# Optimization experiments

Measured on AMD Instinct MI355X. Metric: run time of the kernel, lower is better.

Reference implementation:

```python
import jax, jax.numpy as jnp
import numpy as np

N_NODES = 50000
N_EDGES = 800000
IN_DIM = 64
HID = 64
N_CLASSES = 10
NUM_GRAPHS = 512
EPS = 1e-5


def setup_inputs() -> dict:
    key = jax.random.key(0)
    ks = jax.random.split(key, 24)
    def w(k, shape, fan_in):
        return jax.random.normal(k, shape, jnp.float32) / np.sqrt(fan_in)
    inp = {
        "input_feature": jax.random.normal(ks[0], (N_NODES, IN_DIM), jnp.float32),
        "edge_src": jax.random.randint(ks[1], (N_EDGES,), 0, N_NODES, jnp.int32),
        "edge_dst": jax.random.randint(ks[2], (N_EDGES,), 0, N_NODES, jnp.int32),
        "graph_indicator": jnp.sort(jax.random.randint(ks[3], (N_NODES,), 0, NUM_GRAPHS, jnp.int32)),
        "labels": jax.random.randint(ks[4], (NUM_GRAPHS,), 0, N_CLASSES, jnp.int32),
        # GraphSAGE layer weights (self + neighbor paths) and biases
        "Ws1": w(ks[5], (IN_DIM, HID), IN_DIM), "Wn1": w(ks[6], (IN_DIM, HID), IN_DIM), "b1": jnp.zeros((HID,), jnp.float32),
        "Ws2": w(ks[7], (HID, HID), HID), "Wn2": w(ks[8], (HID, HID), HID), "b2": jnp.zeros((HID,), jnp.float32),
        "Ws3": w(ks[9], (HID, HID), HID), "Wn3": w(ks[10], (HID, HID), HID), "b3": jnp.zeros((HID,), jnp.float32),
        # BatchNorm affine params (bn1 output is discarded by the original forward, so omitted)
        "g2": jnp.ones((HID,), jnp.float32), "be2": jnp.zeros((HID,), jnp.float32),
        "g3": jnp.ones((HID,), jnp.float32), "be3": jnp.zeros((HID,), jnp.float32),
        # MLP head
        "fcW1": w(ks[11], (HID, 2 * HID), HID), "fcb1": jnp.zeros((2 * HID,), jnp.float32),
        "fcW2": w(ks[12], (2 * HID, HID), 2 * HID), "fcb2": jnp.zeros((HID,), jnp.float32),
        "fcW3": w(ks[13], (HID, N_CLASSES), HID), "fcb3": jnp.zeros((N_CLASSES,), jnp.float32),
    }
    return inp


def _batchnorm(x, g, b):
    # training-mode BN over the node dimension
    m = jnp.mean(x, axis=0)
    v = jnp.var(x, axis=0)
    return (x - m) * jax.lax.rsqrt(v + EPS) * g + b


def _sage(x, Ws, Wn, b, src, dst, inv_deg):
    # mean-aggregate neighbor features: agg[i] = mean_{(j->i) in E} x[j]
    msg = x[src]                                                   # [E, d] gather
    agg = jax.ops.segment_sum(msg, dst, num_segments=N_NODES)       # [N, d] scatter-add
    agg = agg * inv_deg                                             # mean aggregation
    return jax.nn.relu(x @ Ws + agg @ Wn + b)


def reference(input_feature, edge_src, edge_dst, graph_indicator, labels,
              Ws1, Wn1, b1, Ws2, Wn2, b2, Ws3, Wn3, b3,
              g2, be2, g3, be3, fcW1, fcb1, fcW2, fcb2, fcW3, fcb3):
    deg = jax.ops.segment_sum(jnp.ones((N_EDGES,), jnp.float32), edge_dst, num_segments=N_NODES)
    inv_deg = (1.0 / jnp.maximum(deg, 1.0))[:, None]                # [N, 1]
    # NOTE: original forward computes bn1(input_feature) but discards it (dead code)
    h = _sage(input_feature, Ws1, Wn1, b1, edge_src, edge_dst, inv_deg)
    h = _batchnorm(h, g2, be2)
    h = _sage(h, Ws2, Wn2, b2, edge_src, edge_dst, inv_deg)
    h = _batchnorm(h, g3, be3)
    h = _sage(h, Ws3, Wn3, b3, edge_src, edge_dst, inv_deg)
    # sum-pool per graph (labels only determine the number of graphs)
    pooled = jax.ops.segment_sum(h, graph_indicator, num_segments=NUM_GRAPHS)  # [G, HID]
    h = jax.nn.relu(pooled @ fcW1 + fcb1)
    h = jax.nn.relu(h @ fcW2 + fcb2)
    logits = h @ fcW3 + fcb3                                        # [G, num_classes]
    return logits
```

## Files before the change

### kernel.cpp

```cpp
#include <hip/hip_runtime.h>

#define N_NODES   50000
#define N_EDGES   800000
#define DIM       64
#define NUM_GRAPHS 512
#define EPS       1e-5f

#define SB   1024
#define NSB  ((N_NODES + SB - 1) / SB)

__global__ void k_zero(int* __restrict__ deg, float* __restrict__ sums2,
                       float* __restrict__ sums3, float* __restrict__ pooled) {
    int i = blockIdx.x * 256 + threadIdx.x;
    if (i < N_NODES) deg[i] = 0;
    if (i < 128) { sums2[i] = 0.f; sums3[i] = 0.f; }
    if (i < NUM_GRAPHS * DIM) pooled[i] = 0.f;
}

__global__ void k_count(const int* __restrict__ dst, int* __restrict__ deg) {
    int i = blockIdx.x * 256 + threadIdx.x;
    if (i < N_EDGES) atomicAdd(&deg[dst[i]], 1);
}

__global__ void __launch_bounds__(1024)
k_scan1(const int* __restrict__ deg, int* __restrict__ bsum) {
    __shared__ int red[16];
    int t = threadIdx.x;
    int i = blockIdx.x * SB + t;
    int v = (i < N_NODES) ? deg[i] : 0;
#pragma unroll
    for (int d = 32; d; d >>= 1) v += __shfl_down(v, d, 64);
    if ((t & 63) == 0) red[t >> 6] = v;
    __syncthreads();
    if (t < 16) {
        int s = red[t];
#pragma unroll
        for (int d = 8; d; d >>= 1) s += __shfl_down(s, d, 16);
        if (t == 0) bsum[blockIdx.x] = s;
    }
}

__global__ void k_scan2(const int* __restrict__ bsum, int* __restrict__ boff) {
    int t = threadIdx.x;
    int v = (t < NSB) ? bsum[t] : 0;
    int orig = v;
#pragma unroll
    for (int d = 1; d < 64; d <<= 1) {
        int u = __shfl_up(v, d, 64);
        if (t >= d) v += u;
    }
    if (t < NSB) boff[t] = v - orig;
}

__global__ void __launch_bounds__(1024)
k_scan3(const int* __restrict__ deg, const int* __restrict__ boff,
        int* __restrict__ off, int* __restrict__ cursor, float* __restrict__ invd) {
    __shared__ int wsum[16];
    int t = threadIdx.x, lane = t & 63, w = t >> 6;
    int i = blockIdx.x * SB + t;
    int d = (i < N_NODES) ? deg[i] : 0;
    int v = d;
#pragma unroll
    for (int s = 1; s < 64; s <<= 1) {
        int u = __shfl_up(v, s, 64);
        if (lane >= s) v += u;
    }
    if (lane == 63) wsum[w] = v;
    __syncthreads();
    if (t < 16) {
        int x = wsum[t];
#pragma unroll
        for (int s = 1; s < 16; s <<= 1) {
            int u = __shfl_up(x, s, 16);
            if (t >= s) x += u;
        }
        wsum[t] = x;
    }
    __syncthreads();
    if (i < N_NODES) {
        int ex = boff[blockIdx.x] + ((w > 0) ? wsum[w - 1] : 0) + v - d;
        off[i] = ex;
        cursor[i] = ex;
        invd[i] = 1.0f / (float)max(d, 1);
        if (i == N_NODES - 1) off[N_NODES] = ex + d;
    }
}

__global__ void k_scatter(const int* __restrict__ src, const int* __restrict__ dst,
                          int* __restrict__ cursor, int* __restrict__ csr_src) {
    int i = blockIdx.x * 256 + threadIdx.x;
    if (i < N_EDGES) {
        int p = atomicAdd(&cursor[dst[i]], 1);
        csr_src[p] = src[i];
    }
}

#define GR 32
template<bool BN>
__global__ void __launch_bounds__(256, 3)
k_gemm(const float* __restrict__ x, const float* __restrict__ Ws,
       const float* __restrict__ Wn, const float* __restrict__ bias,
       const float* __restrict__ bn_a, const float* __restrict__ bn_c,
       float* __restrict__ xs, float* __restrict__ xn) {
    __shared__ float sX[GR][DIM];
    int tid = threadIdx.x;
    int lane = tid & 63, w = tid >> 6;

    float wsr[DIM], wnr[DIM];
#pragma unroll
    for (int k = 0; k < DIM; ++k) {
        wsr[k] = Ws[k * DIM + lane];
        wnr[k] = Wn[k * DIM + lane];
    }
    float bv = bias[lane];
    float aL = 1.f, cL = 0.f;
    if constexpr (BN) { aL = bn_a[lane]; cL = bn_c[lane]; }

    int rowBase = blockIdx.x * GR;
#pragma unroll
    for (int r = 0; r < GR / 4; ++r) {
        int row = r * 4 + w;
        int gr = rowBase + row;
        float v = (gr < N_NODES) ? x[gr * DIM + lane] : 0.f;
        sX[row][lane] = fmaf(v, aL, cL);
    }
    __syncthreads();

#pragma unroll
    for (int r = 0; r < 8; ++r) {
        int row = w * 8 + r;
        float s = bv, n = 0.f;
#pragma unroll
        for (int kg = 0; kg < DIM / 4; ++kg) {
            float4 xv = *reinterpret_cast<const float4*>(&sX[row][kg * 4]);
            s = fmaf(xv.x, wsr[kg * 4 + 0], s); n = fmaf(xv.x, wnr[kg * 4 + 0], n);
            s = fmaf(xv.y, wsr[kg * 4 + 1], s); n = fmaf(xv.y, wnr[kg * 4 + 1], n);
            s = fmaf(xv.z, wsr[kg * 4 + 2], s); n = fmaf(xv.z, wnr[kg * 4 + 2], n);
            s = fmaf(xv.w, wsr[kg * 4 + 3], s); n = fmaf(xv.w, wnr[kg * 4 + 3], n);
        }
        int grow = rowBase + row;
        if (grow < N_NODES) {
            xs[grow * DIM + lane] = s;
            xn[grow * DIM + lane] = n;
        }
    }
}

template<bool POOL>
__global__ void __launch_bounds__(256)
k_agg(const float* __restrict__ xs, const float* __restrict__ xn,
      const int* __restrict__ off, const int* __restrict__ csr_src,
      const float* __restrict__ inv_deg, const int* __restrict__ gind,
      float* __restrict__ h, float* __restrict__ pooled) {
    int lane = threadIdx.x & 63, w = threadIdx.x >> 6;
    int row = blockIdx.x * 4 + w;
    if (row >= N_NODES) return;
    int jb = off[row], je = off[row + 1];
    float acc = 0.f;
    int j = jb;
    for (; j + 4 <= je; j += 4) {
        int i0 = csr_src[j], i1 = csr_src[j + 1], i2 = csr_src[j + 2], i3 = csr_src[j + 3];
        float v0 = xn[i0 * DIM + lane];
        float v1 = xn[i1 * DIM + lane];
        float v2 = xn[i2 * DIM + lane];
        float v3 = xn[i3 * DIM + lane];
        acc += (v0 + v1) + (v2 + v3);
    }
    for (; j < je; ++j) acc += xn[csr_src[j] * DIM + lane];
    float val = fmaf(acc, inv_deg[row], xs[row * DIM + lane]);
    val = fmaxf(val, 0.f);
    h[row * DIM + lane] = val;
    if constexpr (POOL) {
        int g = gind[row];
        atomicAdd(&pooled[g * DIM + lane], val);
    }
}

__global__ void __launch_bounds__(256)
k_stats(const float* __restrict__ h, float* __restrict__ sums) {
    int lane = threadIdx.x & 63, w = threadIdx.x >> 6;
    float s = 0.f, q = 0.f;
    for (int r = blockIdx.x * 4 + w; r < N_NODES; r += gridDim.x * 4) {
        float v = h[r * DIM + lane];
        s += v;
        q = fmaf(v, v, q);
    }
    __shared__ float sS[4][DIM], sQ[4][DIM];
    sS[w][lane] = s; sQ[w][lane] = q;
    __syncthreads();
    if (w == 0) {
        float ts = sS[0][lane] + sS[1][lane] + sS[2][lane] + sS[3][lane];
        float tq = sQ[0][lane] + sQ[1][lane] + sQ[2][lane] + sQ[3][lane];
        atomicAdd(&sums[lane], ts);
        atomicAdd(&sums[DIM + lane], tq);
    }
}

__global__ void k_bnfin(const float* __restrict__ sums, const float* __restrict__ g,
                        const float* __restrict__ be, float* __restrict__ a,
                        float* __restrict__ c) {
    int t = threadIdx.x;
    float m = sums[t] * (1.0f / N_NODES);
    float q = sums[DIM + t] * (1.0f / N_NODES);
    float v = q - m * m;
    float inv = 1.0f / sqrtf(v + EPS);
    float av = g[t] * inv;
    a[t] = av;
    c[t] = be[t] - m * av;
}

__global__ void __launch_bounds__(128)
k_mlp(const float* __restrict__ pooled,
      const float* __restrict__ W1, const float* __restrict__ b1,
      const float* __restrict__ W2, const float* __restrict__ b2,
      const float* __restrict__ W3, const float* __restrict__ b3,
      float* __restrict__ out) {
    __shared__ float sp[64], s1[128], s2[64];
    int g = blockIdx.x, t = threadIdx.x;
    if (t < 64) sp[t] = pooled[g * 64 + t];
    __syncthreads();
    {
        float acc = b1[t];
#pragma unroll
        for (int k = 0; k < 64; ++k) acc = fmaf(sp[k], W1[k * 128 + t], acc);
        s1[t] = fmaxf(acc, 0.f);
    }
    __syncthreads();
    if (t < 64) {
        float acc = b2[t];
#pragma unroll
        for (int k = 0; k < 128; ++k) acc = fmaf(s1[k], W2[k * 64 + t], acc);
        s2[t] = fmaxf(acc, 0.f);
    }
    __syncthreads();
    if (t < 10) {
        float acc = b3[t];
#pragma unroll
        for (int k = 0; k < 64; ++k) acc = fmaf(s2[k], W3[k * 10 + t], acc);
        out[g * 10 + t] = acc;
    }
}

extern "C" void kernel_launch(void* const* d_in, const int* in_sizes, int n_in,
                              void* d_out, int out_size, void* d_ws, size_t ws_size,
                              hipStream_t stream) {
    const float* x0   = (const float*)d_in[0];
    const int* e_src  = (const int*)d_in[1];
    const int* e_dst  = (const int*)d_in[2];
    const int* gind   = (const int*)d_in[3];
    const float* Ws1 = (const float*)d_in[5],  *Wn1 = (const float*)d_in[6],  *b1 = (const float*)d_in[7];
    const float* Ws2 = (const float*)d_in[8],  *Wn2 = (const float*)d_in[9],  *b2 = (const float*)d_in[10];
    const float* Ws3 = (const float*)d_in[11], *Wn3 = (const float*)d_in[12], *b3 = (const float*)d_in[13];
    const float* g2  = (const float*)d_in[14], *be2 = (const float*)d_in[15];
    const float* g3  = (const float*)d_in[16], *be3 = (const float*)d_in[17];
    const float* fcW1 = (const float*)d_in[18], *fcb1 = (const float*)d_in[19];
    const float* fcW2 = (const float*)d_in[20], *fcb2 = (const float*)d_in[21];
    const float* fcW3 = (const float*)d_in[22], *fcb3 = (const float*)d_in[23];
    float* out = (float*)d_out;

    char* p = (char*)d_ws;
    auto carve = [&](size_t bytes) { void* r = (void*)p; p += (bytes + 255) & ~(size_t)255; return r; };
    int*   deg     = (int*)  carve(N_NODES * 4);
    int*   off     = (int*)  carve((N_NODES + 1) * 4);
    int*   cursor  = (int*)  carve(N_NODES * 4);
    int*   csr_src = (int*)  carve(N_EDGES * 4);
    float* invd    = (float*)carve(N_NODES * 4);
    int*   bsum    = (int*)  carve(NSB * 4);
    int*   boff    = (int*)  carve((NSB + 1) * 4);
    float* sums2   = (float*)carve(128 * 4);
    float* sums3   = (float*)carve(128 * 4);
    float* a2      = (float*)carve(64 * 4);
    float* c2      = (float*)carve(64 * 4);
    float* a3      = (float*)carve(64 * 4);
    float* c3      = (float*)carve(64 * 4);
    float* pooled  = (float*)carve(NUM_GRAPHS * DIM * 4);
    float* bufH    = (float*)carve((size_t)N_NODES * DIM * 4);
    float* bufXS   = (float*)carve((size_t)N_NODES * DIM * 4);
    float* bufXN   = (float*)carve((size_t)N_NODES * DIM * 4);

    const int EB = (N_EDGES + 255) / 256;
    const int GB = (N_NODES + GR - 1) / GR;
    const int AB = (N_NODES + 3) / 4;

    k_zero<<<(N_NODES + 255) / 256, 256, 0, stream>>>(deg, sums2, sums3, pooled);
    k_count<<<EB, 256, 0, stream>>>(e_dst, deg);
    k_scan1<<<NSB, SB, 0, stream>>>(deg, bsum);
    k_scan2<<<1, 64, 0, stream>>>(bsum, boff);
    k_scan3<<<NSB, SB, 0, stream>>>(deg, boff, off, cursor, invd);
    k_scatter<<<EB, 256, 0, stream>>>(e_src, e_dst, cursor, csr_src);

    k_gemm<false><<<GB, 256, 0, stream>>>(x0, Ws1, Wn1, b1, nullptr, nullptr, bufXS, bufXN);
    k_agg<false><<<AB, 256, 0, stream>>>(bufXS, bufXN, off, csr_src, invd, nullptr, bufH, nullptr);

    k_stats<<<120, 256, 0, stream>>>(bufH, sums2);
    k_bnfin<<<1, 64, 0, stream>>>(sums2, g2, be2, a2, c2);
    k_gemm<true><<<GB, 256, 0, stream>>>(bufH, Ws2, Wn2, b2, a2, c2, bufXS, bufXN);
    k_agg<false><<<AB, 256, 0, stream>>>(bufXS, bufXN, off, csr_src, invd, nullptr, bufH, nullptr);

    k_stats<<<120, 256, 0, stream>>>(bufH, sums3);
    k_bnfin<<<1, 64, 0, stream>>>(sums3, g3, be3, a3, c3);
    k_gemm<true><<<GB, 256, 0, stream>>>(bufH, Ws3, Wn3, b3, a3, c3, bufXS, bufXN);
    k_agg<true><<<AB, 256, 0, stream>>>(bufXS, bufXN, off, csr_src, invd, gind, bufH, pooled);

    k_mlp<<<NUM_GRAPHS, 128, 0, stream>>>(pooled, fcW1, fcb1, fcW2, fcb2, fcW3, fcb3, out);
}
```

Baseline: 354.3 us.

## Two-pass bucketed CSR scatter for locality; double stats grid size

Replaces the single random scatter that builds CSR with two passes: edges are first binned into 32-node buckets, using bucket cursors seeded from the CSR offsets, then placed per node from the bucketed order. The aim is to make the second pass's cursor atomics and csr_src writes more local, so there is less scattered memory traffic. The cost is an extra kernel, a second read and write of the edge arrays, and temporary storage that reuses the GEMM buffers. It also doubles the k_stats grid from 120 to 240 blocks.

```diff
diff --git a/kernel.cpp b/kernel.cpp
--- a/kernel.cpp
+++ b/kernel.cpp
@@ -8,6 +8,9 @@
 
 #define SB   1024
 #define NSB  ((N_NODES + SB - 1) / SB)
+
+#define BSH  5
+#define NBK  ((N_NODES + 31) / 32)
 
 __global__ void k_zero(int* __restrict__ deg, float* __restrict__ sums2,
                        float* __restrict__ sums3, float* __restrict__ pooled) {
@@ -86,12 +89,29 @@
     }
 }
 
-__global__ void k_scatter(const int* __restrict__ src, const int* __restrict__ dst,
-                          int* __restrict__ cursor, int* __restrict__ csr_src) {
+__global__ void k_binit(const int* __restrict__ off, int* __restrict__ bcur) {
+    int b = blockIdx.x * 256 + threadIdx.x;
+    if (b < NBK) bcur[b] = off[b << BSH];
+}
+
+__global__ void k_bscatter(const int* __restrict__ src, const int* __restrict__ dst,
+                           int* __restrict__ bcur, int* __restrict__ ebs,
+                           int* __restrict__ ebd) {
     int i = blockIdx.x * 256 + threadIdx.x;
     if (i < N_EDGES) {
-        int p = atomicAdd(&cursor[dst[i]], 1);
-        csr_src[p] = src[i];
+        int d = dst[i];
+        int p = atomicAdd(&bcur[d >> BSH], 1);
+        ebs[p] = src[i];
+        ebd[p] = d;
+    }
+}
+
+__global__ void k_scatter2(const int* __restrict__ ebs, const int* __restrict__ ebd,
+                           int* __restrict__ cursor, int* __restrict__ csr_src) {
+    int i = blockIdx.x * 256 + threadIdx.x;
+    if (i < N_EDGES) {
+        int q = atomicAdd(&cursor[ebd[i]], 1);
+        csr_src[q] = ebs[i];
     }
 }
 
@@ -267,6 +287,7 @@
     float* invd    = (float*)carve(N_NODES * 4);
     int*   bsum    = (int*)  carve(NSB * 4);
     int*   boff    = (int*)  carve((NSB + 1) * 4);
+    int*   bcur    = (int*)  carve(NBK * 4);
     float* sums2   = (float*)carve(128 * 4);
     float* sums3   = (float*)carve(128 * 4);
     float* a2      = (float*)carve(64 * 4);
@@ -278,6 +299,9 @@
     float* bufXS   = (float*)carve((size_t)N_NODES * DIM * 4);
     float* bufXN   = (float*)carve((size_t)N_NODES * DIM * 4);
 
+    int* ebs = (int*)bufXS;
+    int* ebd = (int*)bufXN;
+
     const int EB = (N_EDGES + 255) / 256;
     const int GB = (N_NODES + GR - 1) / GR;
     const int AB = (N_NODES + 3) / 4;
@@ -287,17 +311,19 @@
     k_scan1<<<NSB, SB, 0, stream>>>(deg, bsum);
     k_scan2<<<1, 64, 0, stream>>>(bsum, boff);
     k_scan3<<<NSB, SB, 0, stream>>>(deg, boff, off, cursor, invd);
-    k_scatter<<<EB, 256, 0, stream>>>(e_src, e_dst, cursor, csr_src);
+    k_binit<<<(NBK + 255) / 256, 256, 0, stream>>>(off, bcur);
+    k_bscatter<<<EB, 256, 0, stream>>>(e_src, e_dst, bcur, ebs, ebd);
+    k_scatter2<<<EB, 256, 0, stream>>>(ebs, ebd, cursor, csr_src);
 
     k_gemm<false><<<GB, 256, 0, stream>>>(x0, Ws1, Wn1, b1, nullptr, nullptr, bufXS, bufXN);
     k_agg<false><<<AB, 256, 0, stream>>>(bufXS, bufXN, off, csr_src, invd, nullptr, bufH, nullptr);
 
-    k_stats<<<120, 256, 0, stream>>>(bufH, sums2);
+    k_stats<<<240, 256, 0, stream>>>(bufH, sums2);
     k_bnfin<<<1, 64, 0, stream>>>(sums2, g2, be2, a2, c2);
     k_gemm<true><<<GB, 256, 0, stream>>>(bufH, Ws2, Wn2, b2, a2, c2, bufXS, bufXN);
     k_agg<false><<<AB, 256, 0, stream>>>(bufXS, bufXN, off, csr_src, invd, nullptr, bufH, nullptr);
 
-    k_stats<<<120, 256, 0, stream>>>(bufH, sums3);
+    k_stats<<<240, 256, 0, stream>>>(bufH, sums3);
     k_bnfin<<<1, 64, 0, stream>>>(sums3, g3, be3, a3, c3);
     k_gemm<true><<<GB, 256, 0, stream>>>(bufH, Ws3, Wn3, b3, a3, c3, bufXS, bufXN);
     k_agg<true><<<AB, 256, 0, stream>>>(bufXS, bufXN, off, csr_src, invd, gind, bufH, pooled);
```

Measured after the change: 441.3 us. +24.5%, slower.

## Store neighbor-projected features as bf16 and split aggregation across half-wavefronts

Applied to the files above, without the earlier changes.

The neighbor-path GEMM output is packed to bf16 pairs (round-to-nearest-even) so each gathered row is 128 bytes instead of 256, halving the random gather traffic in aggregation. The aggregation kernel now lets each half-wavefront process alternate edges with 32 lanes each loading one packed pair, then combines the halves with a cross-lane shuffle. The stats kernel grid is also doubled. This trades precision in the aggregated neighbor features for lower memory bandwidth in the dominant gather.

```diff
diff --git a/kernel.cpp b/kernel.cpp
--- a/kernel.cpp
+++ b/kernel.cpp
@@ -95,13 +95,18 @@
     }
 }
 
+__device__ inline unsigned f2bf(float f) {
+    unsigned u = __float_as_uint(f);
+    return (u + 0x7FFFu + ((u >> 16) & 1u)) >> 16;
+}
+
 #define GR 32
 template<bool BN>
 __global__ void __launch_bounds__(256, 3)
 k_gemm(const float* __restrict__ x, const float* __restrict__ Ws,
        const float* __restrict__ Wn, const float* __restrict__ bias,
        const float* __restrict__ bn_a, const float* __restrict__ bn_c,
-       float* __restrict__ xs, float* __restrict__ xn) {
+       float* __restrict__ xs, unsigned* __restrict__ xnh) {
     __shared__ float sX[GR][DIM];
     int tid = threadIdx.x;
     int lane = tid & 63, w = tid >> 6;
@@ -139,40 +144,51 @@
             s = fmaf(xv.w, wsr[kg * 4 + 3], s); n = fmaf(xv.w, wnr[kg * 4 + 3], n);
         }
         int grow = rowBase + row;
+        float nOther = __shfl_xor(n, 1, 64);
         if (grow < N_NODES) {
             xs[grow * DIM + lane] = s;
-            xn[grow * DIM + lane] = n;
+            if (!(lane & 1)) {
+                unsigned word = (f2bf(nOther) << 16) | f2bf(n);
+                xnh[grow * 32 + (lane >> 1)] = word;
+            }
         }
     }
 }
 
 template<bool POOL>
 __global__ void __launch_bounds__(256)
-k_agg(const float* __restrict__ xs, const float* __restrict__ xn,
+k_agg(const float* __restrict__ xs, const unsigned* __restrict__ xnh,
       const int* __restrict__ off, const int* __restrict__ csr_src,
       const float* __restrict__ inv_deg, const int* __restrict__ gind,
       float* __restrict__ h, float* __restrict__ pooled) {
-    int lane = threadIdx.x & 63, w = threadIdx.x >> 6;
+    int tid = threadIdx.x;
+    int w = tid >> 6;
+    int lane = tid & 63;
+    int hw = lane >> 5;
+    int p = lane & 31;
     int row = blockIdx.x * 4 + w;
     if (row >= N_NODES) return;
     int jb = off[row], je = off[row + 1];
-    float acc = 0.f;
-    int j = jb;
-    for (; j + 4 <= je; j += 4) {
-        int i0 = csr_src[j], i1 = csr_src[j + 1], i2 = csr_src[j + 2], i3 = csr_src[j + 3];
-        float v0 = xn[i0 * DIM + lane];
-        float v1 = xn[i1 * DIM + lane];
-        float v2 = xn[i2 * DIM + lane];
-        float v3 = xn[i3 * DIM + lane];
-        acc += (v0 + v1) + (v2 + v3);
-    }
-    for (; j < je; ++j) acc += xn[csr_src[j] * DIM + lane];
-    float val = fmaf(acc, inv_deg[row], xs[row * DIM + lane]);
-    val = fmaxf(val, 0.f);
-    h[row * DIM + lane] = val;
-    if constexpr (POOL) {
-        int g = gind[row];
-        atomicAdd(&pooled[g * DIM + lane], val);
+    float ax = 0.f, ay = 0.f;
+    for (int j = jb + hw; j < je; j += 2) {
+        int s = csr_src[j];
+        unsigned wd = xnh[s * 32 + p];
+        ax += __uint_as_float(wd << 16);
+        ay += __uint_as_float(wd & 0xFFFF0000u);
+    }
+    ax += __shfl_xor(ax, 32, 64);
+    ay += __shfl_xor(ay, 32, 64);
+    if (hw == 0) {
+        float id = inv_deg[row];
+        float2 xv = *reinterpret_cast<const float2*>(&xs[row * DIM + 2 * p]);
+        float vx = fmaxf(fmaf(ax, id, xv.x), 0.f);
+        float vy = fmaxf(fmaf(ay, id, xv.y), 0.f);
+        *reinterpret_cast<float2*>(&h[row * DIM + 2 * p]) = make_float2(vx, vy);
+        if constexpr (POOL) {
+            int g = gind[row];
+            atomicAdd(&pooled[g * DIM + 2 * p], vx);
+            atomicAdd(&pooled[g * DIM + 2 * p + 1], vy);
+        }
     }
 }
 
@@ -276,7 +292,7 @@
     float* pooled  = (float*)carve(NUM_GRAPHS * DIM * 4);
     float* bufH    = (float*)carve((size_t)N_NODES * DIM * 4);
     float* bufXS   = (float*)carve((size_t)N_NODES * DIM * 4);
-    float* bufXN   = (float*)carve((size_t)N_NODES * DIM * 4);
+    unsigned* bufXN = (unsigned*)carve((size_t)N_NODES * 32 * 4);
 
     const int EB = (N_EDGES + 255) / 256;
     const int GB = (N_NODES + GR - 1) / GR;
@@ -292,12 +308,12 @@
     k_gemm<false><<<GB, 256, 0, stream>>>(x0, Ws1, Wn1, b1, nullptr, nullptr, bufXS, bufXN);
     k_agg<false><<<AB, 256, 0, stream>>>(bufXS, bufXN, off, csr_src, invd, nullptr, bufH, nullptr);
 
-    k_stats<<<120, 256, 0, stream>>>(bufH, sums2);
+    k_stats<<<240, 256, 0, stream>>>(bufH, sums2);
     k_bnfin<<<1, 64, 0, stream>>>(sums2, g2, be2, a2, c2);
     k_gemm<true><<<GB, 256, 0, stream>>>(bufH, Ws2, Wn2, b2, a2, c2, bufXS, bufXN);
     k_agg<false><<<AB, 256, 0, stream>>>(bufXS, bufXN, off, csr_src, invd, nullptr, bufH, nullptr);
 
-    k_stats<<<120, 256, 0, stream>>>(bufH, sums3);
+    k_stats<<<240, 256, 0, stream>>>(bufH, sums3);
     k_bnfin<<<1, 64, 0, stream>>>(sums3, g3, be3, a3, c3);
     k_gemm<true><<<GB, 256, 0, stream>>>(bufH, Ws3, Wn3, b3, a3, c3, bufXS, bufXN);
     k_agg<true><<<AB, 256, 0, stream>>>(bufXS, bufXN, off, csr_src, invd, gind, bufH, pooled);
```

Measured after the change: 660.2 us. +86.3%, slower.
